# Kernel tuning notes

Hardware: AMD Instinct MI355X
Metric: run time of the kernel (lower is better)

Reference implementation:

```python
import jax, jax.numpy as jnp
import numpy as np

N_NODES = 100000
N_EDGES = 1600000
D_IN = 64
D_OUT = 64
BN_EPS = 1e-5


def setup_inputs() -> dict:
    key = jax.random.key(0)
    k_x, k_src, k_dst, k_ew, k_w = jax.random.split(key, 5)
    x = jax.random.normal(k_x, (N_NODES, D_IN), dtype=jnp.float32)
    edge_src = jax.random.randint(k_src, (N_EDGES,), 0, N_NODES, dtype=jnp.int32)
    edge_dst = jax.random.randint(k_dst, (N_EDGES,), 0, N_NODES, dtype=jnp.int32)
    edge_weight = jax.random.uniform(k_ew, (N_EDGES,), dtype=jnp.float32)
    # Xavier-uniform weight, zero bias (reset_parameters)
    limit = float(np.sqrt(6.0 / (D_IN + D_OUT)))
    W = jax.random.uniform(k_w, (D_IN, D_OUT), dtype=jnp.float32, minval=-limit, maxval=limit)
    bias = jnp.zeros((D_OUT,), dtype=jnp.float32)
    gamma = jnp.ones((D_OUT,), dtype=jnp.float32)
    beta = jnp.zeros((D_OUT,), dtype=jnp.float32)
    return {"x": x, "edge_src": edge_src, "edge_dst": edge_dst,
            "edge_weight": edge_weight, "W": W, "bias": bias,
            "gamma": gamma, "beta": beta}


def reference(x, edge_src, edge_dst, edge_weight, W, bias, gamma, beta):
    # GraphConvolution: support = x @ W  -> [N, D_OUT]
    support = jnp.matmul(x, W)
    # spmm(adj, support) with adj in COO form: out[d] += w_e * support[s]
    msgs = edge_weight[:, None] * support[edge_src]        # [E, D_OUT]
    agg = jax.ops.segment_sum(msgs, edge_dst, num_segments=N_NODES)
    out = agg + bias
    # BatchNorm1d (training mode: batch statistics over node dim)
    mean = jnp.mean(out, axis=0)
    var = jnp.var(out, axis=0)
    out = (out - mean) * jax.lax.rsqrt(var + BN_EPS) * gamma + beta
    # ReLU activation; dropout is identity in deterministic/inference mode
    return jax.nn.relu(out)
```

## Files before the change

kernel.cpp:

```cpp
#include <hip/hip_runtime.h>
#include <hip/hip_bf16.h>

#define NN 100000
#define NE 1600000
#define DD 64
#define NCOARSE 392
#define GEMM_TILES 1563
#define PLACE_EPB 8192
#define PLACE_BLOCKS 196
#define LCNT_STRIDE 200
#define STAT_BLOCKS 256

__device__ inline unsigned short f2bf(float f) {
    __hip_bfloat16 h = __float2bfloat16(f);
    unsigned short s; __builtin_memcpy(&s, &h, 2); return s;
}
__device__ inline float pw(unsigned p) { return __uint_as_float((p & 0xFFFE0000u) >> 1); }

__global__ __launch_bounds__(256) void k_hist(const int* __restrict__ edst,
                                              int* __restrict__ lcntT) {
    __shared__ int h[NCOARSE];
    for (int i = threadIdx.x; i < NCOARSE; i += 256) h[i] = 0;
    __syncthreads();
    const int e0 = blockIdx.x * PLACE_EPB;
#pragma unroll
    for (int k = 0; k < 32; ++k) {
        int e = e0 + k * 256 + threadIdx.x;
        if (e < NE) atomicAdd(&h[edst[e] >> 8], 1);
    }
    __syncthreads();
    for (int i = threadIdx.x; i < NCOARSE; i += 256)
        lcntT[i * LCNT_STRIDE + blockIdx.x] = h[i];
}

__global__ __launch_bounds__(256) void k_colscan(int* __restrict__ lcntT,
                                                 int* __restrict__ cnt) {
    int* col = lcntT + blockIdx.x * LCNT_STRIDE;
    const int t = threadIdx.x;
    const int v = (t < PLACE_BLOCKS) ? col[t] : 0;
    __shared__ int sc[256];
    sc[t] = v; __syncthreads();
    for (int o = 1; o < 256; o <<= 1) {
        int u = (t >= o) ? sc[t - o] : 0;
        __syncthreads();
        sc[t] += u;
        __syncthreads();
    }
    if (t < PLACE_BLOCKS) col[t] = sc[t] - v;
    if (t == 255) cnt[blockIdx.x] = sc[255];
}

__global__ __launch_bounds__(512) void k_scan392(const int* __restrict__ cnt,
                                                 int* __restrict__ cstart,
                                                 int* __restrict__ bstart) {
    __shared__ int sc[512];
    const int t = threadIdx.x;
    const int v = (t < NCOARSE) ? cnt[t] : 0;
    sc[t] = v; __syncthreads();
    for (int o = 1; o < 512; o <<= 1) {
        int u = (t >= o) ? sc[t - o] : 0;
        __syncthreads();
        sc[t] += u;
        __syncthreads();
    }
    if (t < NCOARSE) cstart[t] = sc[t] - v;
    if (t == 0) { cstart[NCOARSE] = NE; bstart[NN] = NE; }
}

__global__ __launch_bounds__(256) void k_gemm_scatter(const float* __restrict__ x,
                                                      const float* __restrict__ Wg,
                                                      unsigned* __restrict__ support2,
                                                      const int* __restrict__ esrc,
                                                      const int* __restrict__ edst,
                                                      const float* __restrict__ ew,
                                                      const int* __restrict__ cstart,
                                                      const int* __restrict__ lcntT,
                                                      int2* __restrict__ permA) {
    if (blockIdx.x < PLACE_BLOCKS) {
        const int blk = blockIdx.x;
        __shared__ int loff[NCOARSE];
        for (int i = threadIdx.x; i < NCOARSE; i += 256)
            loff[i] = cstart[i] + lcntT[i * LCNT_STRIDE + blk];
        __syncthreads();
        const int e0 = blk * PLACE_EPB;
#pragma unroll
        for (int k = 0; k < 32; ++k) {
            int e = e0 + k * 256 + threadIdx.x;
            if (e < NE) {
                int d = edst[e];
                int p = atomicAdd(&loff[d >> 8], 1);
                permA[p] = make_int2(esrc[e] | ((d & 255) << 17), __float_as_int(ew[e]));
            }
        }
        return;
    }

    __shared__ float Ws[DD * DD];
    __shared__ float Xs[64 * DD];
    const int r0 = (blockIdx.x - PLACE_BLOCKS) * 64;
    const int nrows = (r0 + 64 <= NN) ? 64 : (NN - r0);

    for (int i = threadIdx.x; i < DD * DD / 4; i += 256)
        ((float4*)Ws)[i] = ((const float4*)Wg)[i];
    const float4* xg = (const float4*)(x + (size_t)r0 * DD);
    for (int i = threadIdx.x; i < nrows * 16; i += 256)
        ((float4*)Xs)[i] = xg[i];
    __syncthreads();

    const int wave = threadIdx.x >> 6, lane = threadIdx.x & 63;
    const int half = lane >> 5, hl = lane & 31;
    const int rbase = wave * 16 + half * 8;

    float acc0[8] = {0.f, 0.f, 0.f, 0.f, 0.f, 0.f, 0.f, 0.f};
    float acc1[8] = {0.f, 0.f, 0.f, 0.f, 0.f, 0.f, 0.f, 0.f};
#pragma unroll 4
    for (int k = 0; k < DD; k += 4) {
        float2 w0 = *(const float2*)&Ws[(k + 0) * DD + 2 * hl];
        float2 w1 = *(const float2*)&Ws[(k + 1) * DD + 2 * hl];
        float2 w2 = *(const float2*)&Ws[(k + 2) * DD + 2 * hl];
        float2 w3 = *(const float2*)&Ws[(k + 3) * DD + 2 * hl];
#pragma unroll
        for (int r = 0; r < 8; ++r) {
            float4 xv = *(const float4*)&Xs[(rbase + r) * DD + k];
            acc0[r] = fmaf(xv.x, w0.x, acc0[r]); acc1[r] = fmaf(xv.x, w0.y, acc1[r]);
            acc0[r] = fmaf(xv.y, w1.x, acc0[r]); acc1[r] = fmaf(xv.y, w1.y, acc1[r]);
            acc0[r] = fmaf(xv.z, w2.x, acc0[r]); acc1[r] = fmaf(xv.z, w2.y, acc1[r]);
            acc0[r] = fmaf(xv.w, w3.x, acc0[r]); acc1[r] = fmaf(xv.w, w3.y, acc1[r]);
        }
    }
#pragma unroll
    for (int r = 0; r < 8; ++r) {
        const int row = rbase + r;
        if (row < nrows) {
            unsigned p = (unsigned)f2bf(acc0[r]) | ((unsigned)f2bf(acc1[r]) << 16);
            support2[(size_t)(r0 + row) * 32 + hl] = p;
        }
    }
}

__global__ __launch_bounds__(1024) void k_placeB(const int* __restrict__ cstart,
                                                 const int2* __restrict__ permA,
                                                 unsigned* __restrict__ perm,
                                                 int* __restrict__ bstart) {
    __shared__ int sc[256], loff[256], wtot[4];
    const int c = blockIdx.x, t = threadIdx.x;
    const int wave = t >> 6, lane = t & 63;
    const int cs = cstart[c], ce = cstart[c + 1];
    if (t < 256) sc[t] = 0;
    __syncthreads();
    for (int j = cs + t; j < ce; j += 1024)
        atomicAdd(&sc[(permA[j].x >> 17) & 255], 1);
    __syncthreads();
    int v = 0, xv = 0;
    if (wave < 4) {
        v = sc[t];
        xv = v;
#pragma unroll
        for (int o = 1; o < 64; o <<= 1) {
            int u = __shfl_up(xv, o, 64);
            if (lane >= o) xv += u;
        }
        if (lane == 63) wtot[wave] = xv;
    }
    __syncthreads();
    if (t < 4) {
        int w = wtot[t], xw = w;
#pragma unroll
        for (int o = 1; o < 4; o <<= 1) {
            int u = __shfl_up(xw, o, 64);
            if (t >= o) xw += u;
        }
        wtot[t] = xw - w;
    }
    __syncthreads();
    if (wave < 4) {
        const int base = cs + wtot[wave] + xv - v;
        loff[t] = base;
        const int node = c * 256 + t;
        if (node < NN) bstart[node] = base;
    }
    __syncthreads();
    for (int j = cs + t; j < ce; j += 1024) {
        int2 m = permA[j];
        int p = atomicAdd(&loff[(m.x >> 17) & 255], 1);
        unsigned wb = (unsigned)(f2bf(__int_as_float(m.y)) & 0x7FFF);
        perm[p] = (unsigned)(m.x & 0x1FFFF) | (wb << 17);
    }
}

__global__ __launch_bounds__(512) void k_gather(const int* __restrict__ bstart,
                                                const unsigned* __restrict__ perm,
                                                const uint4* __restrict__ support4,
                                                float* __restrict__ out) {
    const int wave = threadIdx.x >> 6, lane = threadIdx.x & 63;
    const int sub = lane >> 3, q = lane & 7;
    const int d = blockIdx.x * 8 + wave;
    const int bs = bstart[d], be = bstart[d + 1];
    float acc[8] = {0.f, 0.f, 0.f, 0.f, 0.f, 0.f, 0.f, 0.f};
    int j0 = bs;
    for (; j0 + 15 < be; j0 += 16) {
        unsigned mA = perm[j0 + sub];
        unsigned mB = perm[j0 + 8 + sub];
        uint4 pA = support4[(size_t)(mA & 0x1FFFF) * 8 + q];
        uint4 pB = support4[(size_t)(mB & 0x1FFFF) * 8 + q];
        float wA = pw(mA), wB = pw(mB);
        acc[0] = fmaf(wA, __uint_as_float(pA.x << 16), acc[0]);
        acc[1] = fmaf(wA, __uint_as_float(pA.x & 0xffff0000u), acc[1]);
        acc[2] = fmaf(wA, __uint_as_float(pA.y << 16), acc[2]);
        acc[3] = fmaf(wA, __uint_as_float(pA.y & 0xffff0000u), acc[3]);
        acc[4] = fmaf(wA, __uint_as_float(pA.z << 16), acc[4]);
        acc[5] = fmaf(wA, __uint_as_float(pA.z & 0xffff0000u), acc[5]);
        acc[6] = fmaf(wA, __uint_as_float(pA.w << 16), acc[6]);
        acc[7] = fmaf(wA, __uint_as_float(pA.w & 0xffff0000u), acc[7]);
        acc[0] = fmaf(wB, __uint_as_float(pB.x << 16), acc[0]);
        acc[1] = fmaf(wB, __uint_as_float(pB.x & 0xffff0000u), acc[1]);
        acc[2] = fmaf(wB, __uint_as_float(pB.y << 16), acc[2]);
        acc[3] = fmaf(wB, __uint_as_float(pB.y & 0xffff0000u), acc[3]);
        acc[4] = fmaf(wB, __uint_as_float(pB.z << 16), acc[4]);
        acc[5] = fmaf(wB, __uint_as_float(pB.z & 0xffff0000u), acc[5]);
        acc[6] = fmaf(wB, __uint_as_float(pB.w << 16), acc[6]);
        acc[7] = fmaf(wB, __uint_as_float(pB.w & 0xffff0000u), acc[7]);
    }
    for (; j0 < be; j0 += 8) {
        if (j0 + sub < be) {
            unsigned m = perm[j0 + sub];
            uint4 p = support4[(size_t)(m & 0x1FFFF) * 8 + q];
            float w = pw(m);
            acc[0] = fmaf(w, __uint_as_float(p.x << 16), acc[0]);
            acc[1] = fmaf(w, __uint_as_float(p.x & 0xffff0000u), acc[1]);
            acc[2] = fmaf(w, __uint_as_float(p.y << 16), acc[2]);
            acc[3] = fmaf(w, __uint_as_float(p.y & 0xffff0000u), acc[3]);
            acc[4] = fmaf(w, __uint_as_float(p.z << 16), acc[4]);
            acc[5] = fmaf(w, __uint_as_float(p.z & 0xffff0000u), acc[5]);
            acc[6] = fmaf(w, __uint_as_float(p.w << 16), acc[6]);
            acc[7] = fmaf(w, __uint_as_float(p.w & 0xffff0000u), acc[7]);
        }
    }
#pragma unroll
    for (int i = 0; i < 8; ++i) {
        acc[i] += __shfl_xor(acc[i], 8, 64);
        acc[i] += __shfl_xor(acc[i], 16, 64);
        acc[i] += __shfl_xor(acc[i], 32, 64);
    }
    if (sub == 0) {
        float* op = out + (size_t)d * DD + q * 8;
        *(float4*)op = make_float4(acc[0], acc[1], acc[2], acc[3]);
        *(float4*)(op + 4) = make_float4(acc[4], acc[5], acc[6], acc[7]);
    }
}

__device__ inline float4 shfl_down4(float4 v, int dd) {
    v.x = __shfl_down(v.x, dd, 64); v.y = __shfl_down(v.y, dd, 64);
    v.z = __shfl_down(v.z, dd, 64); v.w = __shfl_down(v.w, dd, 64);
    return v;
}
__device__ inline float4 add4(float4 a, float4 b) {
    a.x += b.x; a.y += b.y; a.z += b.z; a.w += b.w; return a;
}

__global__ __launch_bounds__(256) void k_stats(const float* __restrict__ agg,
                                               float* __restrict__ pstat) {
    const int lane = threadIdx.x & 63, wave = threadIdx.x >> 6;
    const int q = lane & 15, sub = lane >> 4;
    float4 s = {0, 0, 0, 0}, sq = {0, 0, 0, 0};
    const int stride = gridDim.x * 16;
    for (int row = (blockIdx.x * 4 + wave) * 4 + sub; row < NN; row += stride) {
        float4 v = *(const float4*)(agg + (size_t)row * DD + q * 4);
        s.x += v.x; s.y += v.y; s.z += v.z; s.w += v.w;
        sq.x = fmaf(v.x, v.x, sq.x); sq.y = fmaf(v.y, v.y, sq.y);
        sq.z = fmaf(v.z, v.z, sq.z); sq.w = fmaf(v.w, v.w, sq.w);
    }
    s = add4(s, shfl_down4(s, 32));  s = add4(s, shfl_down4(s, 16));
    sq = add4(sq, shfl_down4(sq, 32)); sq = add4(sq, shfl_down4(sq, 16));

    __shared__ float red[2][4][DD];
    if (lane < 16) {
        red[0][wave][q * 4 + 0] = s.x;  red[0][wave][q * 4 + 1] = s.y;
        red[0][wave][q * 4 + 2] = s.z;  red[0][wave][q * 4 + 3] = s.w;
        red[1][wave][q * 4 + 0] = sq.x; red[1][wave][q * 4 + 1] = sq.y;
        red[1][wave][q * 4 + 2] = sq.z; red[1][wave][q * 4 + 3] = sq.w;
    }
    __syncthreads();
    if (threadIdx.x < 2 * DD) {
        const int t = threadIdx.x;
        const int part = t >> 6, c = t & 63;
        pstat[blockIdx.x * 2 * DD + t] =
            red[part][0][c] + red[part][1][c] + red[part][2][c] + red[part][3][c];
    }
}

__global__ __launch_bounds__(128) void k_finstats(const float* __restrict__ pstat,
                                                  float* __restrict__ ss,
                                                  const float* __restrict__ gamma,
                                                  const float* __restrict__ beta) {
    const int t = threadIdx.x;
    float acc = 0.f;
    for (int b = 0; b < STAT_BLOCKS; ++b)
        acc += pstat[b * 2 * DD + t];
    __shared__ float red[2 * DD];
    red[t] = acc;
    __syncthreads();
    if (t < DD) {
        const float invn = 1.0f / NN;
        float mean = red[t] * invn;
        float var = fmaxf(red[DD + t] * invn - mean * mean, 0.f);
        float sc = rsqrtf(var + 1e-5f) * gamma[t];
        ss[t] = sc;
        ss[DD + t] = beta[t] - mean * sc;
    }
}

__global__ __launch_bounds__(256) void k_final(float* __restrict__ out,
                                               const float* __restrict__ ss) {
    const size_t idx = ((size_t)blockIdx.x * 256 + threadIdx.x) * 4;
    const int c = (int)(idx & 63);
    float4 v = *(const float4*)(out + idx);
    float4 o;
    o.x = fmaxf(fmaf(v.x, ss[c + 0], ss[DD + c + 0]), 0.f);
    o.y = fmaxf(fmaf(v.y, ss[c + 1], ss[DD + c + 1]), 0.f);
    o.z = fmaxf(fmaf(v.z, ss[c + 2], ss[DD + c + 2]), 0.f);
    o.w = fmaxf(fmaf(v.w, ss[c + 3], ss[DD + c + 3]), 0.f);
    *(float4*)(out + idx) = o;
}

extern "C" void kernel_launch(void* const* d_in, const int* in_sizes, int n_in,
                              void* d_out, int out_size, void* d_ws, size_t ws_size,
                              hipStream_t stream) {
    const float* x     = (const float*)d_in[0];
    const int*   esrc  = (const int*)d_in[1];
    const int*   edst  = (const int*)d_in[2];
    const float* ew    = (const float*)d_in[3];
    const float* W     = (const float*)d_in[4];
    const float* gamma = (const float*)d_in[6];
    const float* beta  = (const float*)d_in[7];
    float*       out   = (float*)d_out;

    char* ws = (char*)d_ws;
    unsigned* support2 = (unsigned*)ws;  ws += (size_t)NN * DD * 2;
    int2*     permA  = (int2*)ws;     ws += (size_t)NE * 8;
    unsigned* perm   = (unsigned*)ws; ws += (size_t)NE * 4;
    int*   lcntT  = (int*)ws;    ws += NCOARSE * LCNT_STRIDE * 4;
    int*   cnt    = (int*)ws;    ws += NCOARSE * 4;
    float* ss     = (float*)ws;  ws += 128 * 4;
    int*   cstart = (int*)ws;    ws += (NCOARSE + 1) * 4;
    int*   bstart = (int*)ws;    ws += (NN + 4) * 4;
    float* pstat  = (float*)ws;  ws += STAT_BLOCKS * 2 * DD * 4;

    k_hist        <<<PLACE_BLOCKS, 256, 0, stream>>>(edst, lcntT);
    k_colscan     <<<NCOARSE, 256, 0, stream>>>(lcntT, cnt);
    k_scan392     <<<1, 512, 0, stream>>>(cnt, cstart, bstart);
    k_gemm_scatter<<<PLACE_BLOCKS + GEMM_TILES, 256, 0, stream>>>(
                      x, W, support2, esrc, edst, ew, cstart, lcntT, permA);
    k_placeB      <<<NCOARSE, 1024, 0, stream>>>(cstart, permA, perm, bstart);
    k_gather      <<<NN / 8, 512, 0, stream>>>(bstart, perm, (const uint4*)support2, out);
    k_stats       <<<STAT_BLOCKS, 256, 0, stream>>>(out, pstat);
    k_finstats    <<<1, 128, 0, stream>>>(pstat, ss, gamma, beta);
    k_final       <<<NN * DD / 4 / 256, 256, 0, stream>>>(out, ss);
}
```

Measured before the change: 220.9 us.

## Restructure GEMM tile: wave-uniform W scalar loads, swizzled X LDS, coalesced stores

The dense x@W part of the fused kernel no longer stages W in LDS. Each wave owns 16 output columns and reads W through wave-uniform addresses, which the compiler can turn into scalar loads. Each lane computes one full row from an XOR-swizzled X tile to avoid bank conflicts. Results are repacked through rotated LDS into 16-byte coalesced global stores. This cuts LDS traffic and store transactions, in exchange for more scalar-load pressure and extra barriers.

```diff
diff --git a/kernel.cpp b/kernel.cpp
--- a/kernel.cpp
+++ b/kernel.cpp
@@ -95,45 +95,65 @@
         return;
     }
 
-    __shared__ float Ws[DD * DD];
     __shared__ float Xs[64 * DD];
     const int r0 = (blockIdx.x - PLACE_BLOCKS) * 64;
     const int nrows = (r0 + 64 <= NN) ? 64 : (NN - r0);
-
-    for (int i = threadIdx.x; i < DD * DD / 4; i += 256)
-        ((float4*)Ws)[i] = ((const float4*)Wg)[i];
+    const int t = threadIdx.x;
+
     const float4* xg = (const float4*)(x + (size_t)r0 * DD);
-    for (int i = threadIdx.x; i < nrows * 16; i += 256)
-        ((float4*)Xs)[i] = xg[i];
-    __syncthreads();
-
-    const int wave = threadIdx.x >> 6, lane = threadIdx.x & 63;
-    const int half = lane >> 5, hl = lane & 31;
-    const int rbase = wave * 16 + half * 8;
-
-    float acc0[8] = {0.f, 0.f, 0.f, 0.f, 0.f, 0.f, 0.f, 0.f};
-    float acc1[8] = {0.f, 0.f, 0.f, 0.f, 0.f, 0.f, 0.f, 0.f};
+    for (int i = t; i < nrows * 16; i += 256) {
+        const int row = i >> 4, k4 = i & 15;
+        *(float4*)&Xs[row * 64 + ((k4 ^ (row & 15)) << 2)] = xg[i];
+    }
+    if (nrows < 64) {
+        for (int i = nrows * 16 + t; i < 64 * 16; i += 256)
+            ((float4*)Xs)[i] = make_float4(0.f, 0.f, 0.f, 0.f);
+    }
+    __syncthreads();
+
+    const int lane = t & 63;
+    const int w = __builtin_amdgcn_readfirstlane(t >> 6);
+    const float* Wp = Wg + w * 16;
+
+    float acc[16];
+#pragma unroll
+    for (int c = 0; c < 16; ++c) acc[c] = 0.f;
+
 #pragma unroll 4
-    for (int k = 0; k < DD; k += 4) {
-        float2 w0 = *(const float2*)&Ws[(k + 0) * DD + 2 * hl];
-        float2 w1 = *(const float2*)&Ws[(k + 1) * DD + 2 * hl];
-        float2 w2 = *(const float2*)&Ws[(k + 2) * DD + 2 * hl];
-        float2 w3 = *(const float2*)&Ws[(k + 3) * DD + 2 * hl];
-#pragma unroll
-        for (int r = 0; r < 8; ++r) {
-            float4 xv = *(const float4*)&Xs[(rbase + r) * DD + k];
-            acc0[r] = fmaf(xv.x, w0.x, acc0[r]); acc1[r] = fmaf(xv.x, w0.y, acc1[r]);
-            acc0[r] = fmaf(xv.y, w1.x, acc0[r]); acc1[r] = fmaf(xv.y, w1.y, acc1[r]);
-            acc0[r] = fmaf(xv.z, w2.x, acc0[r]); acc1[r] = fmaf(xv.z, w2.y, acc1[r]);
-            acc0[r] = fmaf(xv.w, w3.x, acc0[r]); acc1[r] = fmaf(xv.w, w3.y, acc1[r]);
-        }
-    }
-#pragma unroll
-    for (int r = 0; r < 8; ++r) {
-        const int row = rbase + r;
+    for (int k4 = 0; k4 < 16; ++k4) {
+        const float4 xv = *(const float4*)&Xs[lane * 64 + ((k4 ^ (lane & 15)) << 2)];
+        const float* wr = Wp + k4 * 4 * DD;
+#pragma unroll
+        for (int c = 0; c < 16; ++c) {
+            acc[c] = fmaf(xv.x, wr[c],          acc[c]);
+            acc[c] = fmaf(xv.y, wr[DD + c],     acc[c]);
+            acc[c] = fmaf(xv.z, wr[2 * DD + c], acc[c]);
+            acc[c] = fmaf(xv.w, wr[3 * DD + c], acc[c]);
+        }
+    }
+
+    __syncthreads();
+    unsigned* Us = (unsigned*)Xs;
+#pragma unroll
+    for (int j = 0; j < 8; ++j) {
+        const unsigned p = (unsigned)f2bf(acc[2 * j]) |
+                           ((unsigned)f2bf(acc[2 * j + 1]) << 16);
+        const int cp = 8 * w + j;
+        Us[lane * 32 + ((cp + lane) & 31)] = p;
+    }
+    __syncthreads();
+    uint4* sg = (uint4*)(support2 + (size_t)r0 * 32);
+#pragma unroll
+    for (int it = 0; it < 2; ++it) {
+        const int g4 = t + it * 256;
+        const int row = g4 >> 3, c0 = (g4 & 7) << 2;
         if (row < nrows) {
-            unsigned p = (unsigned)f2bf(acc0[r]) | ((unsigned)f2bf(acc1[r]) << 16);
-            support2[(size_t)(r0 + row) * 32 + hl] = p;
+            uint4 v;
+            v.x = Us[row * 32 + ((c0 + 0 + row) & 31)];
+            v.y = Us[row * 32 + ((c0 + 1 + row) & 31)];
+            v.z = Us[row * 32 + ((c0 + 2 + row) & 31)];
+            v.w = Us[row * 32 + ((c0 + 3 + row) & 31)];
+            sg[g4] = v;
         }
     }
 }
```

Measured after the change: 218.4 us. No clear change (-1.1%).
